# Performance work log

Hardware: AMD Instinct MI355X
Metric: run time of the kernel (lower is better)

The kernel has to match this reference:

```python
import jax, jax.numpy as jnp
import numpy as np

B, C, H, W = 8, 256, 64, 64
CQK = C // 8  # query/key channels = 32


def setup_inputs() -> dict:
    key = jax.random.key(0)
    ks = jax.random.split(key, 9)
    s_in = 1.0 / np.sqrt(C)  # conv2d default init scale (kernel_size=1)
    x = jax.random.normal(ks[0], (B, C, H, W), dtype=jnp.float32)
    Wq = jax.random.uniform(ks[1], (CQK, C), jnp.float32, -s_in, s_in)
    bq = jax.random.uniform(ks[2], (CQK,), jnp.float32, -s_in, s_in)
    Wk = jax.random.uniform(ks[3], (CQK, C), jnp.float32, -s_in, s_in)
    bk = jax.random.uniform(ks[4], (CQK,), jnp.float32, -s_in, s_in)
    Wv = jax.random.uniform(ks[5], (C, C), jnp.float32, -s_in, s_in)
    bv = jax.random.uniform(ks[6], (C,), jnp.float32, -s_in, s_in)
    Wf = jax.random.uniform(ks[7], (C, C), jnp.float32, -s_in, s_in)
    bf = jax.random.uniform(ks[8], (C,), jnp.float32, -s_in, s_in)
    return {"x": x, "Wq": Wq, "bq": bq, "Wk": Wk, "bk": bk,
            "Wv": Wv, "bv": bv, "Wf": Wf, "bf": bf}


def reference(x, Wq, bq, Wk, bk, Wv, bv, Wf, bf):
    b, c, h, w = x.shape
    n = h * w
    xf = x.reshape(b, c, n)  # [B, C, N]  (1x1 conv == channel matmul)
    q = jnp.einsum('oc,bcn->bon', Wq, xf) + bq[None, :, None]  # [B, C/8, N]
    k = jnp.einsum('oc,bcn->bon', Wk, xf) + bk[None, :, None]  # [B, C/8, N]
    v = jnp.einsum('oc,bcn->bon', Wv, xf) + bv[None, :, None]  # [B, C, N]
    # energy[b,i,j] = sum_c q[b,c,i] * k[b,c,j]; no scaling (matches source)
    energy = jnp.einsum('bci,bcj->bij', q, k)  # [B, N, N]
    attn = jax.nn.softmax(energy, axis=-1)
    # out[b,c,i] = sum_j v[b,c,j] * attn[b,i,j]
    out = jnp.einsum('bcj,bij->bci', v, attn)  # [B, C, N]
    out = jnp.einsum('oc,bcn->bon', Wf, out) + bf[None, :, None]
    return out.reshape(b, c, h, w)
```

## Files before the change

### kernel.cpp

```cpp
#include <hip/hip_runtime.h>
#include <hip/hip_bf16.h>

#define BATCH 8
#define CCH   256
#define NPOS  4096
#define CQK   32

typedef __attribute__((ext_vector_type(8))) short short8;
typedef __attribute__((ext_vector_type(4))) float f32x4;

__device__ inline unsigned short f2b(float f) {
    __hip_bfloat16 h = __float2bfloat16(f);
    return *reinterpret_cast<unsigned short*>(&h);
}

__device__ inline size_t qk_addr(int b, int n, int c) {
    return ((((size_t)b * 256 + (n >> 4)) * 4 + (c >> 3)) * 16 + (n & 15)) * 8 + (c & 7);
}
__device__ inline size_t xt_addr(int b, int n, int c) {
    return (((size_t)b * 256 + (n >> 4)) * 8 + (c >> 5)) * 512
           + (((c >> 3) & 3) * 16 + (n & 15)) * 8 + (c & 7);
}
__device__ inline size_t v_addr(int b, int c, int j) {
    return (((((size_t)b * 128 + (j >> 5)) * 16 + (c >> 4)) * 4 + ((j >> 3) & 3)) * 16 + (c & 15)) * 8 + (j & 7);
}
__device__ inline size_t wsw_addr(int og, int c, int ol) {
    return ((size_t)(og * 8 + (c >> 5))) * 512 + (((c >> 3) & 3) * 16 + ol) * 8 + (c & 7);
}

__global__ __launch_bounds__(256, 4)
void prep_kernel(const float* __restrict__ x,
                 const float* __restrict__ Wq, const float* __restrict__ Wk,
                 const float* __restrict__ Wv, const float* __restrict__ Wf,
                 unsigned short* __restrict__ xt, unsigned short* __restrict__ wsw)
{
    const int bid = blockIdx.x;
    const int t   = threadIdx.x;
    if (bid < 2048) {
        __shared__ float xl[64 * 65];
        const int b   = bid >> 8;
        const int rem = bid & 255;
        const int n0  = (rem & 63) * 64;
        const int c0  = (rem >> 6) * 64;
        #pragma unroll
        for (int ch = 0; ch < 4; ++ch) {
            int f  = t + ch * 256;
            int cl = f >> 4, n4 = (f & 15) * 4;
            float4 v = *(const float4*)(x + (size_t)(b * 256 + c0 + cl) * 4096 + n0 + n4);
            xl[cl * 65 + n4 + 0] = v.x;
            xl[cl * 65 + n4 + 1] = v.y;
            xl[cl * 65 + n4 + 2] = v.z;
            xl[cl * 65 + n4 + 3] = v.w;
        }
        __syncthreads();
        #pragma unroll
        for (int e = 0; e < 2; ++e) {
            int f  = t + e * 256;
            int nl = f >> 3, c8 = (f & 7) * 8;
            short8 s;
            #pragma unroll
            for (int j = 0; j < 8; ++j)
                ((unsigned short*)&s)[j] = f2b(xl[(c8 + j) * 65 + nl]);
            *(short8*)(xt + xt_addr(b, n0 + nl, c0 + c8)) = s;
        }
    } else {
        const int og = bid - 2048;
        const float* src; int orow;
        if (og < 2)       { src = Wq; orow = og * 16; }
        else if (og < 4)  { src = Wk; orow = (og - 2) * 16; }
        else if (og < 20) { src = Wv; orow = (og - 4) * 16; }
        else              { src = Wf; orow = (og - 20) * 16; }
        #pragma unroll
        for (int e = 0; e < 16; ++e) {
            int idx = t + e * 256;
            int ol = idx >> 8, c = idx & 255;
            wsw[wsw_addr(og, c, ol)] = f2b(src[(orow + ol) * 256 + c]);
        }
    }
}

__global__ __launch_bounds__(256, 4)
void qkv_kernel(const unsigned short* __restrict__ xt,
                const unsigned short* __restrict__ wsw,
                const float* __restrict__ bq, const float* __restrict__ bk,
                const float* __restrict__ bv,
                unsigned short* __restrict__ qb, unsigned short* __restrict__ kb,
                unsigned short* __restrict__ vb)
{
    const int nt = blockIdx.x;
    const int ot = blockIdx.y;
    const int b  = blockIdx.z;
    const int t  = threadIdx.x;
    const int w  = t >> 6;
    const int q  = (t >> 4) & 3;
    const int ln = t & 15;
    const int lofs = (q * 16 + ln) * 8;

    if (ot == 0) {
        const int og   = w;
        const int cb16 = (w & 1) * 16;
        short8 af[8];
        #pragma unroll
        for (int kk = 0; kk < 8; ++kk)
            af[kk] = *(const short8*)(wsw + (size_t)(og * 8 + kk) * 512 + lofs);
        const float* bias = (w < 2) ? bq : bk;
        const float b0 = bias[cb16 + q * 4 + 0];
        const float b1 = bias[cb16 + q * 4 + 1];
        const float b2 = bias[cb16 + q * 4 + 2];
        const float b3 = bias[cb16 + q * 4 + 3];
        unsigned short* dst = (w < 2) ? qb : kb;
        #pragma unroll
        for (int nq = 0; nq < 4; ++nq) {
            f32x4 acc = {b0, b1, b2, b3};
            const size_t xbase = (size_t)((b * 256 + nt * 4 + nq) * 8) * 512;
            #pragma unroll
            for (int kk = 0; kk < 8; ++kk) {
                short8 bfr = *(const short8*)(xt + xbase + (size_t)kk * 512 + lofs);
                acc = __builtin_amdgcn_mfma_f32_16x16x32_bf16(af[kk], bfr, acc, 0, 0, 0);
            }
            ushort4 s = {f2b(acc[0]), f2b(acc[1]), f2b(acc[2]), f2b(acc[3])};
            *(ushort4*)(dst + qk_addr(b, nt * 64 + nq * 16 + ln, cb16 + q * 4)) = s;
        }
    } else {
        const int cv0 = (ot - 1) * 64;
        short8 af[8];
        const size_t xbase = (size_t)((b * 256 + nt * 4 + w) * 8) * 512;
        #pragma unroll
        for (int kk = 0; kk < 8; ++kk)
            af[kk] = *(const short8*)(xt + xbase + (size_t)kk * 512 + lofs);
        const int jbase = nt * 64 + w * 16;
        #pragma unroll
        for (int oq = 0; oq < 4; ++oq) {
            const int c = cv0 + oq * 16 + ln;
            const float bb = bv[c];
            f32x4 acc = {bb, bb, bb, bb};
            const int og = 4 + (ot - 1) * 4 + oq;
            #pragma unroll
            for (int kk = 0; kk < 8; ++kk) {
                short8 bfr = *(const short8*)(wsw + (size_t)(og * 8 + kk) * 512 + lofs);
                acc = __builtin_amdgcn_mfma_f32_16x16x32_bf16(af[kk], bfr, acc, 0, 0, 0);
            }
            ushort4 s = {f2b(acc[0]), f2b(acc[1]), f2b(acc[2]), f2b(acc[3])};
            *(ushort4*)(vb + v_addr(b, c, jbase + q * 4)) = s;
        }
    }
}

__global__ __launch_bounds__(256, 2)
void attn_kernel(const unsigned short* __restrict__ qb,
                 const unsigned short* __restrict__ kb,
                 const unsigned short* __restrict__ vb,
                 unsigned short* __restrict__ obb)
{
    __shared__ unsigned short plds[2][64][72];
    __shared__ float lred[64];

    const int bid  = blockIdx.x;
    const int b    = bid & 7;
    const int i0   = (bid >> 3) * 64;
    const int t    = threadIdx.x;
    const int w    = t >> 6;
    const int lane = t & 63;
    const int quad = lane >> 4;
    const int ln   = lane & 15;

    const int ibase = i0 + w * 16;
    const int lofs  = (quad * 16 + ln) * 8;

    const short8 qfrag = *(const short8*)(qb + (((size_t)b * 256 + (ibase >> 4)) * 512) + lofs);

    f32x4 acc[4][4];
    #pragma unroll
    for (int it = 0; it < 4; ++it)
        #pragma unroll
        for (int cc = 0; cc < 4; ++cc) acc[it][cc] = (f32x4){0.f, 0.f, 0.f, 0.f};
    float accl[4] = {0.f, 0.f, 0.f, 0.f};

    const unsigned short* kbase = kb + (size_t)b * 256 * 512;
    const unsigned short* vbase = vb + (size_t)b * 128 * 8192;

    short8 kf[4], vf[4][2];
    #pragma unroll
    for (int jc = 0; jc < 4; ++jc)
        kf[jc] = *(const short8*)(kbase + (size_t)jc * 512 + lofs);
    #pragma unroll
    for (int cc = 0; cc < 4; ++cc) {
        vf[cc][0] = *(const short8*)(vbase + (w * 4 + cc) * 512 + lofs);
        vf[cc][1] = *(const short8*)(vbase + 8192 + (w * 4 + cc) * 512 + lofs);
    }

    int pb = 0;
    for (int j0 = 0; j0 < 4096; j0 += 64, pb ^= 1) {
        const int jn = (j0 + 64) & 4095;
        short8 kf_n[4], vf_n[4][2];
        #pragma unroll
        for (int jc = 0; jc < 4; ++jc)
            kf_n[jc] = *(const short8*)(kbase + ((size_t)((jn >> 4) + jc) * 512) + lofs);
        const unsigned short* vt_n = vbase + (size_t)(jn >> 5) * 8192;
        #pragma unroll
        for (int cc = 0; cc < 4; ++cc) {
            vf_n[cc][0] = *(const short8*)(vt_n + (w * 4 + cc) * 512 + lofs);
            vf_n[cc][1] = *(const short8*)(vt_n + 8192 + (w * 4 + cc) * 512 + lofs);
        }
        f32x4 s[4];
        #pragma unroll
        for (int jc = 0; jc < 4; ++jc)
            s[jc] = __builtin_amdgcn_mfma_f32_16x16x32_bf16(qfrag, kf[jc],
                     (f32x4){0.f, 0.f, 0.f, 0.f}, 0, 0, 0);
        #pragma unroll
        for (int jc = 0; jc < 4; ++jc) {
            #pragma unroll
            for (int r = 0; r < 4; ++r) {
                float p = __expf(s[jc][r]);
                accl[r] += p;
                plds[pb][w * 16 + quad * 4 + r][jc * 16 + ln] = f2b(p);
            }
        }
        __syncthreads();
        #pragma unroll
        for (int it = 0; it < 4; ++it) {
            const short8 pf0 = *(const short8*)&plds[pb][it * 16 + ln][quad * 8];
            const short8 pf1 = *(const short8*)&plds[pb][it * 16 + ln][32 + quad * 8];
            #pragma unroll
            for (int cc = 0; cc < 4; ++cc) {
                acc[it][cc] = __builtin_amdgcn_mfma_f32_16x16x32_bf16(pf0, vf[cc][0], acc[it][cc], 0, 0, 0);
                acc[it][cc] = __builtin_amdgcn_mfma_f32_16x16x32_bf16(pf1, vf[cc][1], acc[it][cc], 0, 0, 0);
            }
        }
        #pragma unroll
        for (int jc = 0; jc < 4; ++jc) kf[jc] = kf_n[jc];
        #pragma unroll
        for (int cc = 0; cc < 4; ++cc) {
            vf[cc][0] = vf_n[cc][0];
            vf[cc][1] = vf_n[cc][1];
        }
    }

    #pragma unroll
    for (int r = 0; r < 4; ++r) {
        float v = accl[r];
        v += __shfl_xor(v, 1, 16);
        v += __shfl_xor(v, 2, 16);
        v += __shfl_xor(v, 4, 16);
        v += __shfl_xor(v, 8, 16);
        if (ln == 0) lred[w * 16 + quad * 4 + r] = v;
    }
    __syncthreads();

    #pragma unroll
    for (int it = 0; it < 4; ++it) {
        float linv[4];
        #pragma unroll
        for (int r = 0; r < 4; ++r) linv[r] = 1.f / lred[it * 16 + quad * 4 + r];
        #pragma unroll
        for (int cc = 0; cc < 4; ++cc) {
            const int c = w * 64 + cc * 16 + ln;
            #pragma unroll
            for (int r = 0; r < 4; ++r) {
                const int i = i0 + it * 16 + quad * 4 + r;
                obb[xt_addr(b, i, c)] = f2b(acc[it][cc][r] * linv[r]);
            }
        }
    }
}

__global__ __launch_bounds__(256, 4)
void proj_kernel(const unsigned short* __restrict__ obb,
                 const unsigned short* __restrict__ wsw,
                 const float* __restrict__ bfb, float* __restrict__ out)
{
    const int it = blockIdx.x;
    const int ot = blockIdx.y;
    const int b  = blockIdx.z;
    const int t  = threadIdx.x;
    const int w  = t >> 6;
    const int q  = (t >> 4) & 3;
    const int ln = t & 15;
    const int lofs = (q * 16 + ln) * 8;

    short8 af[8];
    const size_t abase = (size_t)((b * 256 + it * 4 + w) * 8) * 512;
    #pragma unroll
    for (int kk = 0; kk < 8; ++kk)
        af[kk] = *(const short8*)(obb + abase + (size_t)kk * 512 + lofs);

    const int ibase = it * 64 + w * 16;
    #pragma unroll
    for (int oq = 0; oq < 4; ++oq) {
        f32x4 acc = {0.f, 0.f, 0.f, 0.f};
        const int og = 20 + ot * 4 + oq;
        #pragma unroll
        for (int kk = 0; kk < 8; ++kk) {
            short8 bfr = *(const short8*)(wsw + (size_t)(og * 8 + kk) * 512 + lofs);
            acc = __builtin_amdgcn_mfma_f32_16x16x32_bf16(af[kk], bfr, acc, 0, 0, 0);
        }
        const int o = ot * 64 + oq * 16 + ln;
        const float bias = bfb[o];
        float4 s = {acc[0] + bias, acc[1] + bias, acc[2] + bias, acc[3] + bias};
        *(float4*)(out + (size_t)(b * 256 + o) * 4096 + ibase + q * 4) = s;
    }
}

extern "C" void kernel_launch(void* const* d_in, const int* in_sizes, int n_in,
                              void* d_out, int out_size, void* d_ws, size_t ws_size,
                              hipStream_t stream)
{
    const float* x  = (const float*)d_in[0];
    const float* Wq = (const float*)d_in[1];
    const float* bq = (const float*)d_in[2];
    const float* Wk = (const float*)d_in[3];
    const float* bk = (const float*)d_in[4];
    const float* Wv = (const float*)d_in[5];
    const float* bv = (const float*)d_in[6];
    const float* Wf = (const float*)d_in[7];
    const float* bf = (const float*)d_in[8];
    float* out = (float*)d_out;

    unsigned short* xt  = (unsigned short*)d_ws;
    unsigned short* qb  = xt + (size_t)BATCH * NPOS * CCH;
    unsigned short* kb  = qb + (size_t)BATCH * NPOS * CQK;
    unsigned short* vb  = kb + (size_t)BATCH * NPOS * CQK;
    unsigned short* wsw = vb + (size_t)BATCH * CCH * NPOS;
    unsigned short* obb = xt;

    prep_kernel<<<2048 + 36, 256, 0, stream>>>(x, Wq, Wk, Wv, Wf, xt, wsw);
    qkv_kernel<<<dim3(64, 5, 8), 256, 0, stream>>>(xt, wsw, bq, bk, bv, qb, kb, vb);
    attn_kernel<<<512, 256, 0, stream>>>(qb, kb, vb, obb);
    proj_kernel<<<dim3(64, 4, 8), 256, 0, stream>>>(obb, wsw, bf, out);
}
```

Baseline: 213.9 us.

## Fuse x transpose into QKV kernel and output projection into attention kernel

Removes the separate x-to-bf16 transpose pass by having the QKV kernel read fp32 x directly, convert it, and stage fragments in LDS. That block then computes Q, K and all V channels for a 64-position tile. The final 1x1 projection moves into the attention kernel's epilogue: normalized outputs go to a padded LDS tile and are multiplied by Wf there, dropping the obb round trip and one launch. The costs are strided uncoalesced fp32 reads of x in qkv, lower occupancy (launch bounds 2), and extra LDS and register pressure in the attention kernel.

```diff
diff --git a/kernel.cpp b/kernel.cpp
--- a/kernel.cpp
+++ b/kernel.cpp
@@ -17,10 +17,6 @@
 __device__ inline size_t qk_addr(int b, int n, int c) {
     return ((((size_t)b * 256 + (n >> 4)) * 4 + (c >> 3)) * 16 + (n & 15)) * 8 + (c & 7);
 }
-__device__ inline size_t xt_addr(int b, int n, int c) {
-    return (((size_t)b * 256 + (n >> 4)) * 8 + (c >> 5)) * 512
-           + (((c >> 3) & 3) * 16 + (n & 15)) * 8 + (c & 7);
-}
 __device__ inline size_t v_addr(int b, int c, int j) {
     return (((((size_t)b * 128 + (j >> 5)) * 16 + (c >> 4)) * 4 + ((j >> 3) & 3)) * 16 + (c & 15)) * 8 + (j & 7);
 }
@@ -29,119 +25,98 @@
 }
 
 __global__ __launch_bounds__(256, 4)
-void prep_kernel(const float* __restrict__ x,
-                 const float* __restrict__ Wq, const float* __restrict__ Wk,
-                 const float* __restrict__ Wv, const float* __restrict__ Wf,
-                 unsigned short* __restrict__ xt, unsigned short* __restrict__ wsw)
-{
-    const int bid = blockIdx.x;
-    const int t   = threadIdx.x;
-    if (bid < 2048) {
-        __shared__ float xl[64 * 65];
-        const int b   = bid >> 8;
-        const int rem = bid & 255;
-        const int n0  = (rem & 63) * 64;
-        const int c0  = (rem >> 6) * 64;
-        #pragma unroll
-        for (int ch = 0; ch < 4; ++ch) {
-            int f  = t + ch * 256;
-            int cl = f >> 4, n4 = (f & 15) * 4;
-            float4 v = *(const float4*)(x + (size_t)(b * 256 + c0 + cl) * 4096 + n0 + n4);
-            xl[cl * 65 + n4 + 0] = v.x;
-            xl[cl * 65 + n4 + 1] = v.y;
-            xl[cl * 65 + n4 + 2] = v.z;
-            xl[cl * 65 + n4 + 3] = v.w;
-        }
-        __syncthreads();
-        #pragma unroll
-        for (int e = 0; e < 2; ++e) {
-            int f  = t + e * 256;
-            int nl = f >> 3, c8 = (f & 7) * 8;
-            short8 s;
-            #pragma unroll
-            for (int j = 0; j < 8; ++j)
-                ((unsigned short*)&s)[j] = f2b(xl[(c8 + j) * 65 + nl]);
-            *(short8*)(xt + xt_addr(b, n0 + nl, c0 + c8)) = s;
-        }
-    } else {
-        const int og = bid - 2048;
-        const float* src; int orow;
-        if (og < 2)       { src = Wq; orow = og * 16; }
-        else if (og < 4)  { src = Wk; orow = (og - 2) * 16; }
-        else if (og < 20) { src = Wv; orow = (og - 4) * 16; }
-        else              { src = Wf; orow = (og - 20) * 16; }
-        #pragma unroll
-        for (int e = 0; e < 16; ++e) {
-            int idx = t + e * 256;
-            int ol = idx >> 8, c = idx & 255;
-            wsw[wsw_addr(og, c, ol)] = f2b(src[(orow + ol) * 256 + c]);
-        }
-    }
-}
-
-__global__ __launch_bounds__(256, 4)
-void qkv_kernel(const unsigned short* __restrict__ xt,
+void prep_w_kernel(const float* __restrict__ Wq, const float* __restrict__ Wk,
+                   const float* __restrict__ Wv, const float* __restrict__ Wf,
+                   unsigned short* __restrict__ wsw)
+{
+    const int og = blockIdx.x;
+    const int t  = threadIdx.x;
+    const float* src; int orow;
+    if (og < 2)       { src = Wq; orow = og * 16; }
+    else if (og < 4)  { src = Wk; orow = (og - 2) * 16; }
+    else if (og < 20) { src = Wv; orow = (og - 4) * 16; }
+    else              { src = Wf; orow = (og - 20) * 16; }
+    #pragma unroll
+    for (int e = 0; e < 16; ++e) {
+        int idx = t + e * 256;
+        int ol = idx >> 8, c = idx & 255;
+        wsw[wsw_addr(og, c, ol)] = f2b(src[(orow + ol) * 256 + c]);
+    }
+}
+
+__global__ __launch_bounds__(256, 2)
+void qkv_kernel(const float* __restrict__ x,
                 const unsigned short* __restrict__ wsw,
                 const float* __restrict__ bq, const float* __restrict__ bk,
                 const float* __restrict__ bv,
                 unsigned short* __restrict__ qb, unsigned short* __restrict__ kb,
                 unsigned short* __restrict__ vb)
 {
-    const int nt = blockIdx.x;
-    const int ot = blockIdx.y;
-    const int b  = blockIdx.z;
-    const int t  = threadIdx.x;
-    const int w  = t >> 6;
-    const int q  = (t >> 4) & 3;
-    const int ln = t & 15;
+    __shared__ __align__(16) unsigned short xfrag[4][8][512];
+
+    const int nt   = blockIdx.x;
+    const int b    = blockIdx.y;
+    const int t    = threadIdx.x;
+    const int w    = t >> 6;
+    const int lane = t & 63;
+    const int q    = lane >> 4;
+    const int ln   = lane & 15;
     const int lofs = (q * 16 + ln) * 8;
 
-    if (ot == 0) {
-        const int og   = w;
-        const int cb16 = (w & 1) * 16;
-        short8 af[8];
+    {
+        const float* xb = x + ((size_t)b * 256) * 4096 + (nt * 64 + w * 16 + ln);
+        #pragma unroll
+        for (int kk = 0; kk < 8; ++kk) {
+            short8 s;
+            #pragma unroll
+            for (int j = 0; j < 8; ++j)
+                ((unsigned short*)&s)[j] = f2b(xb[(size_t)(kk * 32 + q * 8 + j) * 4096]);
+            *(short8*)&xfrag[w][kk][lane * 8] = s;
+        }
+    }
+    __syncthreads();
+
+    short8 wqk[8];
+    #pragma unroll
+    for (int kk = 0; kk < 8; ++kk)
+        wqk[kk] = *(const short8*)(wsw + (size_t)(w * 8 + kk) * 512 + lofs);
+    const float* bias = (w < 2) ? bq : bk;
+    const int cb16 = (w & 1) * 16;
+    const float b0 = bias[cb16 + q * 4 + 0];
+    const float b1 = bias[cb16 + q * 4 + 1];
+    const float b2 = bias[cb16 + q * 4 + 2];
+    const float b3 = bias[cb16 + q * 4 + 3];
+    unsigned short* dst = (w < 2) ? qb : kb;
+
+    #pragma unroll
+    for (int it = 0; it < 4; ++it) {
+        short8 xf[8];
         #pragma unroll
         for (int kk = 0; kk < 8; ++kk)
-            af[kk] = *(const short8*)(wsw + (size_t)(og * 8 + kk) * 512 + lofs);
-        const float* bias = (w < 2) ? bq : bk;
-        const float b0 = bias[cb16 + q * 4 + 0];
-        const float b1 = bias[cb16 + q * 4 + 1];
-        const float b2 = bias[cb16 + q * 4 + 2];
-        const float b3 = bias[cb16 + q * 4 + 3];
-        unsigned short* dst = (w < 2) ? qb : kb;
-        #pragma unroll
-        for (int nq = 0; nq < 4; ++nq) {
+            xf[kk] = *(const short8*)&xfrag[it][kk][lane * 8];
+
+        {
             f32x4 acc = {b0, b1, b2, b3};
-            const size_t xbase = (size_t)((b * 256 + nt * 4 + nq) * 8) * 512;
-            #pragma unroll
-            for (int kk = 0; kk < 8; ++kk) {
-                short8 bfr = *(const short8*)(xt + xbase + (size_t)kk * 512 + lofs);
-                acc = __builtin_amdgcn_mfma_f32_16x16x32_bf16(af[kk], bfr, acc, 0, 0, 0);
-            }
+            #pragma unroll
+            for (int kk = 0; kk < 8; ++kk)
+                acc = __builtin_amdgcn_mfma_f32_16x16x32_bf16(wqk[kk], xf[kk], acc, 0, 0, 0);
             ushort4 s = {f2b(acc[0]), f2b(acc[1]), f2b(acc[2]), f2b(acc[3])};
-            *(ushort4*)(dst + qk_addr(b, nt * 64 + nq * 16 + ln, cb16 + q * 4)) = s;
-        }
-    } else {
-        const int cv0 = (ot - 1) * 64;
-        short8 af[8];
-        const size_t xbase = (size_t)((b * 256 + nt * 4 + w) * 8) * 512;
-        #pragma unroll
-        for (int kk = 0; kk < 8; ++kk)
-            af[kk] = *(const short8*)(xt + xbase + (size_t)kk * 512 + lofs);
-        const int jbase = nt * 64 + w * 16;
+            *(ushort4*)(dst + qk_addr(b, nt * 64 + it * 16 + ln, cb16 + q * 4)) = s;
+        }
+
         #pragma unroll
         for (int oq = 0; oq < 4; ++oq) {
-            const int c = cv0 + oq * 16 + ln;
+            const int c  = w * 64 + oq * 16 + ln;
             const float bb = bv[c];
             f32x4 acc = {bb, bb, bb, bb};
-            const int og = 4 + (ot - 1) * 4 + oq;
+            const int og = 4 + w * 4 + oq;
             #pragma unroll
             for (int kk = 0; kk < 8; ++kk) {
                 short8 bfr = *(const short8*)(wsw + (size_t)(og * 8 + kk) * 512 + lofs);
-                acc = __builtin_amdgcn_mfma_f32_16x16x32_bf16(af[kk], bfr, acc, 0, 0, 0);
+                acc = __builtin_amdgcn_mfma_f32_16x16x32_bf16(xf[kk], bfr, acc, 0, 0, 0);
             }
             ushort4 s = {f2b(acc[0]), f2b(acc[1]), f2b(acc[2]), f2b(acc[3])};
-            *(ushort4*)(vb + v_addr(b, c, jbase + q * 4)) = s;
+            *(ushort4*)(vb + v_addr(b, c, nt * 64 + it * 16 + q * 4)) = s;
         }
     }
 }
@@ -150,9 +125,10 @@
 void attn_kernel(const unsigned short* __restrict__ qb,
                  const unsigned short* __restrict__ kb,
                  const unsigned short* __restrict__ vb,
-                 unsigned short* __restrict__ obb)
-{
-    __shared__ unsigned short plds[2][64][72];
+                 const unsigned short* __restrict__ wsw,
+                 const float* __restrict__ bfb, float* __restrict__ out)
+{
+    __shared__ __align__(16) unsigned short shbuf[64 * 264];
     __shared__ float lred[64];
 
     const int bid  = blockIdx.x;
@@ -213,14 +189,14 @@
             for (int r = 0; r < 4; ++r) {
                 float p = __expf(s[jc][r]);
                 accl[r] += p;
-                plds[pb][w * 16 + quad * 4 + r][jc * 16 + ln] = f2b(p);
+                shbuf[((size_t)(pb * 64 + w * 16 + quad * 4 + r)) * 72 + jc * 16 + ln] = f2b(p);
             }
         }
         __syncthreads();
         #pragma unroll
         for (int it = 0; it < 4; ++it) {
-            const short8 pf0 = *(const short8*)&plds[pb][it * 16 + ln][quad * 8];
-            const short8 pf1 = *(const short8*)&plds[pb][it * 16 + ln][32 + quad * 8];
+            const short8 pf0 = *(const short8*)&shbuf[((size_t)(pb * 64 + it * 16 + ln)) * 72 + quad * 8];
+            const short8 pf1 = *(const short8*)&shbuf[((size_t)(pb * 64 + it * 16 + ln)) * 72 + 32 + quad * 8];
             #pragma unroll
             for (int cc = 0; cc < 4; ++cc) {
                 acc[it][cc] = __builtin_amdgcn_mfma_f32_16x16x32_bf16(pf0, vf[cc][0], acc[it][cc], 0, 0, 0);
@@ -256,48 +232,32 @@
         for (int cc = 0; cc < 4; ++cc) {
             const int c = w * 64 + cc * 16 + ln;
             #pragma unroll
-            for (int r = 0; r < 4; ++r) {
-                const int i = i0 + it * 16 + quad * 4 + r;
-                obb[xt_addr(b, i, c)] = f2b(acc[it][cc][r] * linv[r]);
-            }
-        }
-    }
-}
-
-__global__ __launch_bounds__(256, 4)
-void proj_kernel(const unsigned short* __restrict__ obb,
-                 const unsigned short* __restrict__ wsw,
-                 const float* __restrict__ bfb, float* __restrict__ out)
-{
-    const int it = blockIdx.x;
-    const int ot = blockIdx.y;
-    const int b  = blockIdx.z;
-    const int t  = threadIdx.x;
-    const int w  = t >> 6;
-    const int q  = (t >> 4) & 3;
-    const int ln = t & 15;
-    const int lofs = (q * 16 + ln) * 8;
-
-    short8 af[8];
-    const size_t abase = (size_t)((b * 256 + it * 4 + w) * 8) * 512;
-    #pragma unroll
-    for (int kk = 0; kk < 8; ++kk)
-        af[kk] = *(const short8*)(obb + abase + (size_t)kk * 512 + lofs);
-
-    const int ibase = it * 64 + w * 16;
-    #pragma unroll
-    for (int oq = 0; oq < 4; ++oq) {
-        f32x4 acc = {0.f, 0.f, 0.f, 0.f};
-        const int og = 20 + ot * 4 + oq;
-        #pragma unroll
-        for (int kk = 0; kk < 8; ++kk) {
-            short8 bfr = *(const short8*)(wsw + (size_t)(og * 8 + kk) * 512 + lofs);
-            acc = __builtin_amdgcn_mfma_f32_16x16x32_bf16(af[kk], bfr, acc, 0, 0, 0);
-        }
-        const int o = ot * 64 + oq * 16 + ln;
-        const float bias = bfb[o];
-        float4 s = {acc[0] + bias, acc[1] + bias, acc[2] + bias, acc[3] + bias};
-        *(float4*)(out + (size_t)(b * 256 + o) * 4096 + ibase + q * 4) = s;
+            for (int r = 0; r < 4; ++r)
+                shbuf[((size_t)(it * 16 + quad * 4 + r)) * 264 + c] = f2b(acc[it][cc][r] * linv[r]);
+        }
+    }
+    __syncthreads();
+
+    #pragma unroll
+    for (int it = 0; it < 4; ++it) {
+        short8 af[8];
+        #pragma unroll
+        for (int kk = 0; kk < 8; ++kk)
+            af[kk] = *(const short8*)&shbuf[((size_t)(it * 16 + ln)) * 264 + kk * 32 + quad * 8];
+        #pragma unroll
+        for (int oq = 0; oq < 4; ++oq) {
+            const int o  = w * 64 + oq * 16 + ln;
+            const int og = 20 + w * 4 + oq;
+            f32x4 pa = {0.f, 0.f, 0.f, 0.f};
+            #pragma unroll
+            for (int kk = 0; kk < 8; ++kk) {
+                short8 bfr = *(const short8*)(wsw + (size_t)(og * 8 + kk) * 512 + lofs);
+                pa = __builtin_amdgcn_mfma_f32_16x16x32_bf16(af[kk], bfr, pa, 0, 0, 0);
+            }
+            const float bias = bfb[o];
+            float4 s = {pa[0] + bias, pa[1] + bias, pa[2] + bias, pa[3] + bias};
+            *(float4*)(out + (size_t)(b * 256 + o) * 4096 + i0 + it * 16 + quad * 4) = s;
+        }
     }
 }
 
@@ -316,15 +276,12 @@
     const float* bf = (const float*)d_in[8];
     float* out = (float*)d_out;
 
-    unsigned short* xt  = (unsigned short*)d_ws;
-    unsigned short* qb  = xt + (size_t)BATCH * NPOS * CCH;
+    unsigned short* qb  = (unsigned short*)d_ws;
     unsigned short* kb  = qb + (size_t)BATCH * NPOS * CQK;
     unsigned short* vb  = kb + (size_t)BATCH * NPOS * CQK;
     unsigned short* wsw = vb + (size_t)BATCH * CCH * NPOS;
-    unsigned short* obb = xt;
-
-    prep_kernel<<<2048 + 36, 256, 0, stream>>>(x, Wq, Wk, Wv, Wf, xt, wsw);
-    qkv_kernel<<<dim3(64, 5, 8), 256, 0, stream>>>(xt, wsw, bq, bk, bv, qb, kb, vb);
-    attn_kernel<<<512, 256, 0, stream>>>(qb, kb, vb, obb);
-    proj_kernel<<<dim3(64, 4, 8), 256, 0, stream>>>(obb, wsw, bf, out);
-}
+
+    prep_w_kernel<<<36, 256, 0, stream>>>(Wq, Wk, Wv, Wf, wsw);
+    qkv_kernel<<<dim3(64, 8), 256, 0, stream>>>(x, wsw, bq, bk, bv, qb, kb, vb);
+    attn_kernel<<<512, 256, 0, stream>>>(qb, kb, vb, wsw, bf, out);
+}
```

Result: no change. 210.3 us (-1.7%).
